# Optimization experiments

Measured on AMD Instinct MI355X. Metric: run time of the kernel, lower is better.

The kernel has to match this reference:

```python
import jax, jax.numpy as jnp
import numpy as np

INPUT_DIM = 1024
OUTPUT_DIM = 512


def setup_inputs() -> dict:
    key = jax.random.key(0)
    ks = jax.random.split(key, 7)
    s_in = 1.0 / np.sqrt(INPUT_DIM)
    x = jax.random.normal(ks[0], (8, 2048, INPUT_DIM), dtype=jnp.float32)
    Wq = jax.random.uniform(ks[1], (INPUT_DIM, INPUT_DIM), jnp.float32, -s_in, s_in)
    bq = jax.random.uniform(ks[2], (INPUT_DIM,), jnp.float32, -s_in, s_in)
    Wk = jax.random.uniform(ks[3], (INPUT_DIM, INPUT_DIM), jnp.float32, -s_in, s_in)
    bk = jax.random.uniform(ks[4], (INPUT_DIM,), jnp.float32, -s_in, s_in)
    Wv = jax.random.uniform(ks[5], (INPUT_DIM, OUTPUT_DIM), jnp.float32, -s_in, s_in)
    bv = jax.random.uniform(ks[6], (OUTPUT_DIM,), jnp.float32, -s_in, s_in)
    return {"x": x, "Wq": Wq, "bq": bq, "Wk": Wk, "bk": bk, "Wv": Wv, "bv": bv}


def reference(x, Wq, bq, Wk, bk, Wv, bv):
    # x: [B, S, D]
    B, S, D = x.shape
    scale = 1.0 / jnp.sqrt(jnp.asarray(D, x.dtype))
    Q = jnp.einsum('bsd,de->bse', x, Wq) + bq  # [B,S,D]
    K = jnp.einsum('bsd,de->bse', x, Wk) + bk  # [B,S,D]
    V = jnp.einsum('bsd,de->bse', x, Wv) + bv  # [B,S,O]
    scores = jnp.einsum('bqd,bkd->bqk', Q, K) * scale  # [B,S,S]
    causal = jnp.tril(jnp.ones((S, S), dtype=bool))
    scores = jnp.where(causal, scores, -jnp.inf)
    attn = jax.nn.softmax(scores, axis=-1)
    return jnp.einsum('bqk,bko->bqo', attn, V)  # [B,S,O]
```

## Files before the change

kernel.cpp:

```cpp
#include <hip/hip_runtime.h>
#include <hip/hip_bf16.h>
#include <stdint.h>
#include <cmath>

typedef __bf16 bf16x8 __attribute__((ext_vector_type(8)));
typedef float f32x4 __attribute__((ext_vector_type(4)));

#define NB 8
#define NS 2048
#define ND 1024
#define NO 512

__device__ __forceinline__ unsigned short f2bf(float f) {
  union { float f; uint32_t u; } c;
  c.f = f;
  uint32_t u = c.u;
  uint32_t r = (u + 0x7fffu + ((u >> 16) & 1u)) >> 16;
  return (unsigned short)r;
}

__device__ __forceinline__ void glds16(const void* g, void* l) {
  __builtin_amdgcn_global_load_lds(
      (const __attribute__((address_space(1))) unsigned int*)g,
      (__attribute__((address_space(3))) unsigned int*)l, 16, 0, 0);
}

__global__ void cast_x_kernel(const float* __restrict__ in,
                              unsigned short* __restrict__ out, int n8) {
  int i = blockIdx.x * blockDim.x + threadIdx.x;
  if (i >= n8) return;
  const float4* p = reinterpret_cast<const float4*>(in) + 2 * (size_t)i;
  float4 a = p[0], b = p[1];
  union { unsigned short us[8]; int4 v; } r;
  r.us[0] = f2bf(a.x); r.us[1] = f2bf(a.y); r.us[2] = f2bf(a.z); r.us[3] = f2bf(a.w);
  r.us[4] = f2bf(b.x); r.us[5] = f2bf(b.y); r.us[6] = f2bf(b.z); r.us[7] = f2bf(b.w);
  reinterpret_cast<int4*>(out)[i] = r.v;
}

__global__ void transpose_cast_kernel(const float* __restrict__ in,
                                      unsigned short* __restrict__ out,
                                      int R, int C) {
  __shared__ unsigned short t[32][33];
  int bx = blockIdx.x;
  int by = blockIdx.y;
  int x = threadIdx.x & 31, y = threadIdx.x >> 5;
#pragma unroll
  for (int j = 0; j < 4; j++) {
    int r = by * 32 + y + j * 8;
    int c = bx * 32 + x;
    t[y + j * 8][x] = f2bf(in[(size_t)r * C + c]);
  }
  __syncthreads();
#pragma unroll
  for (int j = 0; j < 4; j++) {
    int c = bx * 32 + y + j * 8;
    int r = by * 32 + x;
    out[(size_t)c * R + r] = t[x][y + j * 8];
  }
}

__global__ void transpose_v_kernel(const unsigned short* __restrict__ in,
                                   unsigned short* __restrict__ out) {
  __shared__ unsigned short t[32][33];
  int b = blockIdx.z;
  int bo = blockIdx.x;
  int bs = blockIdx.y;
  const unsigned short* ib = in + (size_t)b * NS * NO;
  unsigned short* ob = out + (size_t)b * NO * NS;
  int x = threadIdx.x & 31, y = threadIdx.x >> 5;
#pragma unroll
  for (int j = 0; j < 4; j++)
    t[y + j * 8][x] = ib[(size_t)(bs * 32 + y + j * 8) * NO + bo * 32 + x];
  __syncthreads();
#pragma unroll
  for (int j = 0; j < 4; j++)
    ob[(size_t)(bo * 32 + y + j * 8) * NS + bs * 32 + x] = t[x][y + j * 8];
}

__global__ __launch_bounds__(256, 2) void gemm_bias_kernel(
    const unsigned short* __restrict__ A, const unsigned short* __restrict__ Bt,
    const float* __restrict__ bias, unsigned short* __restrict__ C,
    int M, int N, int K) {
  __shared__ unsigned short lA[128 * 32];
  __shared__ unsigned short lB[128 * 32];
  const int tid = threadIdx.x;
  const int w = tid >> 6, l = tid & 63;
  const int m0 = blockIdx.x * 128, n0 = blockIdx.y * 128;
  const int wr = w >> 1, wc = w & 1;
  const int lr16 = l & 15, lg = l >> 4;
  f32x4 acc[4][4];
#pragma unroll
  for (int i = 0; i < 4; i++)
#pragma unroll
    for (int j = 0; j < 4; j++) acc[i][j] = (f32x4){0.f, 0.f, 0.f, 0.f};
  const int srow = w * 32 + (l >> 2);
  const int sk = (l & 3) * 8;
  for (int k0 = 0; k0 < K; k0 += 32) {
#pragma unroll
    for (int j = 0; j < 2; j++) {
      glds16(&A[(size_t)(m0 + srow + j * 16) * K + k0 + sk], &lA[w * 1024 + j * 512]);
      glds16(&Bt[(size_t)(n0 + srow + j * 16) * K + k0 + sk], &lB[w * 1024 + j * 512]);
    }
    __syncthreads();
    bf16x8 af[4], bfr[4];
#pragma unroll
    for (int mi = 0; mi < 4; mi++)
      af[mi] = *reinterpret_cast<const bf16x8*>(&lA[(wr * 64 + mi * 16 + lr16) * 32 + lg * 8]);
#pragma unroll
    for (int ni = 0; ni < 4; ni++)
      bfr[ni] = *reinterpret_cast<const bf16x8*>(&lB[(wc * 64 + ni * 16 + lr16) * 32 + lg * 8]);
#pragma unroll
    for (int mi = 0; mi < 4; mi++)
#pragma unroll
      for (int ni = 0; ni < 4; ni++)
        acc[mi][ni] = __builtin_amdgcn_mfma_f32_16x16x32_bf16(af[mi], bfr[ni], acc[mi][ni], 0, 0, 0);
    __syncthreads();
  }
#pragma unroll
  for (int ni = 0; ni < 4; ni++) {
    int col = n0 + wc * 64 + ni * 16 + lr16;
    float bv = bias[col];
#pragma unroll
    for (int mi = 0; mi < 4; mi++) {
#pragma unroll
      for (int i = 0; i < 4; i++) {
        int row = m0 + wr * 64 + mi * 16 + lg * 4 + i;
        C[(size_t)row * N + col] = f2bf(acc[mi][ni][i] + bv);
      }
    }
  }
}

__global__ __launch_bounds__(256, 2) void flash_split_kernel(
    const unsigned short* __restrict__ Q, const unsigned short* __restrict__ K,
    const unsigned short* __restrict__ Vt, unsigned short* __restrict__ opart,
    float* __restrict__ ml) {
  __shared__ unsigned short ubuf[3 * 8192];
  __shared__ unsigned short lP[64 * 64];
  const int bid = blockIdx.x;
  const int b = bid & 7;
  const int t = bid >> 3;
  int qi, half;
  if (t < 32) { qi = 31 - (t >> 1); half = t & 1; }
  else        { int u2 = t - 32; qi = u2 >> 1; half = u2 & 1; }
  const int nkt = qi + 1;
  const int h = (qi + 2) >> 1;
  const int lo = half ? h : 0;
  const int hi = half ? nkt : h;
  const int total = 12 * (hi - lo);

  const int tid = threadIdx.x, w = tid >> 6, l = tid & 63;
  const unsigned short* Qb = Q + (size_t)b * NS * ND;
  const unsigned short* Kb = K + (size_t)b * NS * ND;
  const unsigned short* Vb = Vt + (size_t)b * NO * NS;
  const int q0 = qi * 64;
  const int lr16 = l & 15, lg = l >> 4;

  bf16x8 qreg[32];
  {
    const unsigned short* qrow = &Qb[(size_t)(q0 + w * 16 + lr16) * ND + lg * 8];
#pragma unroll
    for (int c = 0; c < 32; c++)
      qreg[c] = *reinterpret_cast<const bf16x8*>(qrow + c * 32);
  }

  f32x4 acc_o[32];
#pragma unroll
  for (int f = 0; f < 32; f++) acc_o[f] = (f32x4){0.f, 0.f, 0.f, 0.f};
  float m_s[4], l_s[4];
#pragma unroll
  for (int i = 0; i < 4; i++) { m_s[i] = -INFINITY; l_s[i] = 0.f; }
  const float sc = 0.03125f * 1.4426950408889634f;

  auto stage = [&](int g) {
    int ki = lo + g / 12, u = g - (g / 12) * 12;
    int k0 = ki * 64;
    unsigned short* dst = &ubuf[(g % 3) * 8192];
    if (u < 8) {
#pragma unroll
      for (int j = 0; j < 4; j++) {
        int row = j * 16 + w * 4 + (l >> 4);
        int gl = (l & 15) ^ (row & 7);
        glds16(&Kb[(size_t)(k0 + row) * ND + u * 128 + gl * 8],
               dst + j * 2048 + w * 512);
      }
    } else {
      int nc = u - 8;
#pragma unroll
      for (int j = 0; j < 4; j++) {
        int row = j * 32 + w * 8 + (l >> 3);
        int gl = (l & 7) ^ (row & 7);
        glds16(&Vb[(size_t)(nc * 128 + row) * NS + k0 + gl * 8],
               dst + j * 2048 + w * 512);
      }
    }
  };

  if (total > 0) {
    stage(0);
    stage(1);

    bf16x8 pa0 = {}, pa1 = {};
    for (int ki = lo; ki < hi; ++ki) {
      const int gbase = (ki - lo) * 12;
      f32x4 accs[4];
#pragma unroll
      for (int f = 0; f < 4; f++) accs[f] = (f32x4){0.f, 0.f, 0.f, 0.f};

#pragma unroll
      for (int u = 0; u < 12; ++u) {
        const int g = gbase + u;
        const bool isLast = (g == total - 1);
        if (!isLast)
          asm volatile("s_waitcnt vmcnt(4) lgkmcnt(0)\ns_barrier" ::: "memory");
        else
          asm volatile("s_waitcnt vmcnt(0) lgkmcnt(0)\ns_barrier" ::: "memory");
        if (g + 2 < total) stage(g + 2);
        const unsigned short* bp = &ubuf[(g % 3) * 8192];

        if (u < 8) {
#pragma unroll
          for (int ks = 0; ks < 4; ks++) {
            bf16x8 a = qreg[u * 4 + ks];
#pragma unroll
            for (int fn = 0; fn < 4; fn++) {
              int row = fn * 16 + lr16;
              int p = (ks * 4 + lg) ^ (row & 7);
              bf16x8 bb = *reinterpret_cast<const bf16x8*>(&bp[row * 128 + p * 8]);
              accs[fn] = __builtin_amdgcn_mfma_f32_16x16x32_bf16(a, bb, accs[fn], 0, 0, 0);
            }
          }
          if (u == 7) {
            const bool diag = (ki == qi);
            float alpha[4];
#pragma unroll
            for (int i = 0; i < 4; i++) {
              float v0 = accs[0][i] * sc, v1 = accs[1][i] * sc;
              float v2 = accs[2][i] * sc, v3 = accs[3][i] * sc;
              if (diag) {
                int qr = w * 16 + lg * 4 + i;
                if (lr16 > qr) v0 = -INFINITY;
                if (16 + lr16 > qr) v1 = -INFINITY;
                if (32 + lr16 > qr) v2 = -INFINITY;
                if (48 + lr16 > qr) v3 = -INFINITY;
              }
              float pm = fmaxf(fmaxf(v0, v1), fmaxf(v2, v3));
              pm = fmaxf(pm, __shfl_xor(pm, 1));
              pm = fmaxf(pm, __shfl_xor(pm, 2));
              pm = fmaxf(pm, __shfl_xor(pm, 4));
              pm = fmaxf(pm, __shfl_xor(pm, 8));
              float mn = fmaxf(m_s[i], pm);
              float al = exp2f(m_s[i] - mn);
              float p0 = exp2f(v0 - mn), p1 = exp2f(v1 - mn);
              float p2 = exp2f(v2 - mn), p3 = exp2f(v3 - mn);
              float rs = (p0 + p1) + (p2 + p3);
              rs += __shfl_xor(rs, 1);
              rs += __shfl_xor(rs, 2);
              rs += __shfl_xor(rs, 4);
              rs += __shfl_xor(rs, 8);
              l_s[i] = l_s[i] * al + rs;
              m_s[i] = mn;
              alpha[i] = al;
              accs[0][i] = p0; accs[1][i] = p1; accs[2][i] = p2; accs[3][i] = p3;
            }
#pragma unroll
            for (int f = 0; f < 32; f++)
#pragma unroll
              for (int i = 0; i < 4; i++) acc_o[f][i] *= alpha[i];
#pragma unroll
            for (int fn = 0; fn < 4; fn++)
#pragma unroll
              for (int i = 0; i < 4; i++) {
                int pr = w * 16 + lg * 4 + i;
                int pg = (fn * 2 + (lr16 >> 3)) ^ (pr & 7);
                lP[pr * 64 + pg * 8 + (lr16 & 7)] = f2bf(accs[fn][i]);
              }
          }
        } else {
          const int nc = u - 8;
          if (u == 8) {
            int prow = w * 16 + lr16;
            pa0 = *reinterpret_cast<const bf16x8*>(&lP[prow * 64 + ((0 + lg) ^ (prow & 7)) * 8]);
            pa1 = *reinterpret_cast<const bf16x8*>(&lP[prow * 64 + ((4 + lg) ^ (prow & 7)) * 8]);
          }
#pragma unroll
          for (int fc = 0; fc < 8; fc++) {
            int row = fc * 16 + lr16;
            int p0i = (0 + lg) ^ (row & 7);
            int p1i = (4 + lg) ^ (row & 7);
            bf16x8 b0 = *reinterpret_cast<const bf16x8*>(&bp[row * 64 + p0i * 8]);
            bf16x8 b1 = *reinterpret_cast<const bf16x8*>(&bp[row * 64 + p1i * 8]);
            int f = nc * 8 + fc;
            acc_o[f] = __builtin_amdgcn_mfma_f32_16x16x32_bf16(pa0, b0, acc_o[f], 0, 0, 0);
            acc_o[f] = __builtin_amdgcn_mfma_f32_16x16x32_bf16(pa1, b1, acc_o[f], 0, 0, 0);
          }
        }
      }
    }
  }

  const int slot = (qi * 2 + half) * 8 + b;
  unsigned short* op = opart + (size_t)slot * 64 * 512;
#pragma unroll
  for (int nc = 0; nc < 4; nc++)
#pragma unroll
    for (int fc = 0; fc < 8; fc++)
#pragma unroll
      for (int i = 0; i < 4; i++) {
        int row = w * 16 + lg * 4 + i;
        int col = nc * 128 + fc * 16 + lr16;
        op[(size_t)row * 512 + col] = f2bf(acc_o[nc * 8 + fc][i]);
      }
  float* mlp = ml + slot * 128;
  if (lr16 == 0) {
#pragma unroll
    for (int i = 0; i < 4; i++) {
      int row = w * 16 + lg * 4 + i;
      mlp[row] = m_s[i];
      mlp[64 + row] = l_s[i];
    }
  }
}

__global__ __launch_bounds__(256) void combine_kernel(
    const unsigned short* __restrict__ opart, const float* __restrict__ ml,
    float* __restrict__ Out) {
  const int bid = blockIdx.x;
  const int b = bid & 7, qi = bid >> 3;
  const int tid = threadIdx.x;
  const int c8 = (tid & 63) * 8;
  const int rbase = (tid >> 6) * 16;
  const int sA = (qi * 2 + 0) * 8 + b;
  const int sB = sA + 8;
  const unsigned short* OA = opart + (size_t)sA * 32768;
  const unsigned short* OB = opart + (size_t)sB * 32768;
  const float* mlA = ml + sA * 128;
  const float* mlB = ml + sB * 128;
  float* ob = Out + ((size_t)b * NS + qi * 64) * NO;
#pragma unroll
  for (int rr = 0; rr < 16; rr++) {
    int r = rbase + rr;
    float mA = mlA[r], lA = mlA[64 + r];
    float mB = mlB[r], lB = mlB[64 + r];
    float m = fmaxf(mA, mB);
    float eA = exp2f(mA - m);
    float eB = (mB == -INFINITY) ? 0.f : exp2f(mB - m);
    float inv = 1.0f / (eA * lA + eB * lB);
    bf16x8 a = *reinterpret_cast<const bf16x8*>(&OA[(size_t)r * 512 + c8]);
    bf16x8 bb = *reinterpret_cast<const bf16x8*>(&OB[(size_t)r * 512 + c8]);
    float4 o0, o1;
    o0.x = ((float)a[0] * eA + (float)bb[0] * eB) * inv;
    o0.y = ((float)a[1] * eA + (float)bb[1] * eB) * inv;
    o0.z = ((float)a[2] * eA + (float)bb[2] * eB) * inv;
    o0.w = ((float)a[3] * eA + (float)bb[3] * eB) * inv;
    o1.x = ((float)a[4] * eA + (float)bb[4] * eB) * inv;
    o1.y = ((float)a[5] * eA + (float)bb[5] * eB) * inv;
    o1.z = ((float)a[6] * eA + (float)bb[6] * eB) * inv;
    o1.w = ((float)a[7] * eA + (float)bb[7] * eB) * inv;
    float4* dst = reinterpret_cast<float4*>(&ob[(size_t)r * 512 + c8]);
    dst[0] = o0;
    dst[1] = o1;
  }
}

extern "C" void kernel_launch(void* const* d_in, const int* in_sizes, int n_in,
                              void* d_out, int out_size, void* d_ws, size_t ws_size,
                              hipStream_t stream) {
  const float* x = (const float*)d_in[0];
  const float* Wq = (const float*)d_in[1];
  const float* bq = (const float*)d_in[2];
  const float* Wk = (const float*)d_in[3];
  const float* bk = (const float*)d_in[4];
  const float* Wv = (const float*)d_in[5];
  const float* bv = (const float*)d_in[6];
  float* out = (float*)d_out;
  char* ws = (char*)d_ws;

  unsigned short* xb  = (unsigned short*)(ws + 0);
  unsigned short* wqt = (unsigned short*)(ws + 33554432);
  unsigned short* wkt = (unsigned short*)(ws + 35651584);
  unsigned short* wvt = (unsigned short*)(ws + 37748736);
  unsigned short* Qb  = (unsigned short*)(ws + 38797312);
  unsigned short* Kb  = (unsigned short*)(ws + 72351744);
  unsigned short* Vb  = (unsigned short*)(ws + 105906176);
  unsigned short* Vtb = (unsigned short*)(ws + 122683392);
  unsigned short* opart = xb;
  float* mlbuf = (float*)(ws + 105906176);

  cast_x_kernel<<<8192, 256, 0, stream>>>(x, xb, (NB * NS * ND) / 8);
  transpose_cast_kernel<<<dim3(32, 32), 256, 0, stream>>>(Wq, wqt, ND, ND);
  transpose_cast_kernel<<<dim3(32, 32), 256, 0, stream>>>(Wk, wkt, ND, ND);
  transpose_cast_kernel<<<dim3(16, 32), 256, 0, stream>>>(Wv, wvt, ND, NO);
  gemm_bias_kernel<<<dim3(128, 8), 256, 0, stream>>>(xb, wqt, bq, Qb, NB * NS, ND, ND);
  gemm_bias_kernel<<<dim3(128, 8), 256, 0, stream>>>(xb, wkt, bk, Kb, NB * NS, ND, ND);
  gemm_bias_kernel<<<dim3(128, 4), 256, 0, stream>>>(xb, wvt, bv, Vb, NB * NS, NO, ND);
  transpose_v_kernel<<<dim3(16, 64, 8), 256, 0, stream>>>(Vb, Vtb);
  flash_split_kernel<<<512, 256, 0, stream>>>(Qb, Kb, Vtb, opart, mlbuf);
  combine_kernel<<<256, 256, 0, stream>>>(opart, mlbuf, out);
}
```

Baseline: 599.6 us.

## Double-buffer GEMM LDS tiles and deepen flash attention prefetch to four stages

The projection GEMM now uses two LDS buffers, so the next K-tile's global-to-LDS load is issued before computing on the current one, hiding load latency behind MFMA work. The flash attention kernel moves from a 3-deep to a 4-deep ring of staging buffers, issuing loads three steps ahead with matching vmcnt waits. It also drops its launch-bounds occupancy hint from 2 to 1 to make room for the extra LDS. The larger LDS footprint in both kernels and the lower occupancy hint may reduce how many blocks run concurrently per CU.

```diff
diff --git a/kernel.cpp b/kernel.cpp
--- a/kernel.cpp
+++ b/kernel.cpp
@@ -81,8 +81,8 @@
     const unsigned short* __restrict__ A, const unsigned short* __restrict__ Bt,
     const float* __restrict__ bias, unsigned short* __restrict__ C,
     int M, int N, int K) {
-  __shared__ unsigned short lA[128 * 32];
-  __shared__ unsigned short lB[128 * 32];
+  __shared__ unsigned short lA[2][128 * 32];
+  __shared__ unsigned short lB[2][128 * 32];
   const int tid = threadIdx.x;
   const int w = tid >> 6, l = tid & 63;
   const int m0 = blockIdx.x * 128, n0 = blockIdx.y * 128;
@@ -95,26 +95,33 @@
     for (int j = 0; j < 4; j++) acc[i][j] = (f32x4){0.f, 0.f, 0.f, 0.f};
   const int srow = w * 32 + (l >> 2);
   const int sk = (l & 3) * 8;
-  for (int k0 = 0; k0 < K; k0 += 32) {
+  auto stage = [&](int buf, int k0) {
 #pragma unroll
     for (int j = 0; j < 2; j++) {
-      glds16(&A[(size_t)(m0 + srow + j * 16) * K + k0 + sk], &lA[w * 1024 + j * 512]);
-      glds16(&Bt[(size_t)(n0 + srow + j * 16) * K + k0 + sk], &lB[w * 1024 + j * 512]);
+      glds16(&A[(size_t)(m0 + srow + j * 16) * K + k0 + sk], &lA[buf][w * 1024 + j * 512]);
+      glds16(&Bt[(size_t)(n0 + srow + j * 16) * K + k0 + sk], &lB[buf][w * 1024 + j * 512]);
     }
-    __syncthreads();
+  };
+  const int nt = K >> 5;
+  stage(0, 0);
+  __syncthreads();
+  int cur = 0;
+  for (int t = 0; t < nt; ++t) {
+    if (t + 1 < nt) stage(cur ^ 1, (t + 1) * 32);
     bf16x8 af[4], bfr[4];
 #pragma unroll
     for (int mi = 0; mi < 4; mi++)
-      af[mi] = *reinterpret_cast<const bf16x8*>(&lA[(wr * 64 + mi * 16 + lr16) * 32 + lg * 8]);
+      af[mi] = *reinterpret_cast<const bf16x8*>(&lA[cur][(wr * 64 + mi * 16 + lr16) * 32 + lg * 8]);
 #pragma unroll
     for (int ni = 0; ni < 4; ni++)
-      bfr[ni] = *reinterpret_cast<const bf16x8*>(&lB[(wc * 64 + ni * 16 + lr16) * 32 + lg * 8]);
+      bfr[ni] = *reinterpret_cast<const bf16x8*>(&lB[cur][(wc * 64 + ni * 16 + lr16) * 32 + lg * 8]);
 #pragma unroll
     for (int mi = 0; mi < 4; mi++)
 #pragma unroll
       for (int ni = 0; ni < 4; ni++)
         acc[mi][ni] = __builtin_amdgcn_mfma_f32_16x16x32_bf16(af[mi], bfr[ni], acc[mi][ni], 0, 0, 0);
     __syncthreads();
+    cur ^= 1;
   }
 #pragma unroll
   for (int ni = 0; ni < 4; ni++) {
@@ -131,11 +138,11 @@
   }
 }
 
-__global__ __launch_bounds__(256, 2) void flash_split_kernel(
+__global__ __launch_bounds__(256, 1) void flash_split_kernel(
     const unsigned short* __restrict__ Q, const unsigned short* __restrict__ K,
     const unsigned short* __restrict__ Vt, unsigned short* __restrict__ opart,
     float* __restrict__ ml) {
-  __shared__ unsigned short ubuf[3 * 8192];
+  __shared__ unsigned short ubuf[4 * 8192];
   __shared__ unsigned short lP[64 * 64];
   const int bid = blockIdx.x;
   const int b = bid & 7;
@@ -175,7 +182,7 @@
   auto stage = [&](int g) {
     int ki = lo + g / 12, u = g - (g / 12) * 12;
     int k0 = ki * 64;
-    unsigned short* dst = &ubuf[(g % 3) * 8192];
+    unsigned short* dst = &ubuf[(g & 3) * 8192];
     if (u < 8) {
 #pragma unroll
       for (int j = 0; j < 4; j++) {
@@ -198,7 +205,8 @@
 
   if (total > 0) {
     stage(0);
-    stage(1);
+    if (total > 1) stage(1);
+    if (total > 2) stage(2);
 
     bf16x8 pa0 = {}, pa1 = {};
     for (int ki = lo; ki < hi; ++ki) {
@@ -210,13 +218,15 @@
 #pragma unroll
       for (int u = 0; u < 12; ++u) {
         const int g = gbase + u;
-        const bool isLast = (g == total - 1);
-        if (!isLast)
+        const int rem = total - g;
+        if (rem > 2)
+          asm volatile("s_waitcnt vmcnt(8) lgkmcnt(0)\ns_barrier" ::: "memory");
+        else if (rem > 1)
           asm volatile("s_waitcnt vmcnt(4) lgkmcnt(0)\ns_barrier" ::: "memory");
         else
           asm volatile("s_waitcnt vmcnt(0) lgkmcnt(0)\ns_barrier" ::: "memory");
-        if (g + 2 < total) stage(g + 2);
-        const unsigned short* bp = &ubuf[(g % 3) * 8192];
+        if (g + 3 < total) stage(g + 3);
+        const unsigned short* bp = &ubuf[(g & 3) * 8192];
 
         if (u < 8) {
 #pragma unroll
```

Result: faster. 487.8 us (-18.6%).
